# Optimization experiments

Measured on AMD Instinct MI355X. Metric: run time of the kernel, lower is better.

The kernel has to match this reference:

```python
import jax, jax.numpy as jnp
import numpy as np

D_MODEL = 512
NUM_HEADS = 8
D_K = D_MODEL // NUM_HEADS


def setup_inputs() -> dict:
    key = jax.random.key(0)
    ks = jax.random.split(key, 9)
    s = 1.0 / np.sqrt(D_MODEL)
    x = jax.random.normal(ks[0], (2, 4096, D_MODEL), dtype=jnp.float32)
    Wq = jax.random.uniform(ks[1], (D_MODEL, D_MODEL), jnp.float32, -s, s)
    bq = jax.random.uniform(ks[2], (D_MODEL,), jnp.float32, -s, s)
    Wk = jax.random.uniform(ks[3], (D_MODEL, D_MODEL), jnp.float32, -s, s)
    bk = jax.random.uniform(ks[4], (D_MODEL,), jnp.float32, -s, s)
    Wv = jax.random.uniform(ks[5], (D_MODEL, D_MODEL), jnp.float32, -s, s)
    bv = jax.random.uniform(ks[6], (D_MODEL,), jnp.float32, -s, s)
    Wo = jax.random.uniform(ks[7], (D_MODEL, D_MODEL), jnp.float32, -s, s)
    bo = jax.random.uniform(ks[8], (D_MODEL,), jnp.float32, -s, s)
    return {"x": x, "Wq": Wq, "bq": bq, "Wk": Wk, "bk": bk,
            "Wv": Wv, "bv": bv, "Wo": Wo, "bo": bo}


def reference(x, Wq, bq, Wk, bk, Wv, bv, Wo, bo):
    B, S, _ = x.shape
    # projections; split heads -> [B, H, S, d_k]
    def heads(t):
        return t.reshape(B, S, NUM_HEADS, D_K).transpose(0, 2, 1, 3)
    Q = heads(x @ Wq + bq)
    K = heads(x @ Wk + bk)
    V = heads(x @ Wv + bv)
    scores = jnp.einsum('bhqd,bhkd->bhqk', Q, K) / jnp.sqrt(jnp.float32(D_K))
    attn = jax.nn.softmax(scores, axis=-1)
    out = jnp.einsum('bhqk,bhkd->bhqd', attn, V)
    out = out.transpose(0, 2, 1, 3).reshape(B, S, D_MODEL)
    return out @ Wo + bo
```

## Files before the change

kernel.cpp:

```cpp
#include <hip/hip_runtime.h>
#include <hip/hip_bf16.h>

#define S_LEN 4096
#define DMODEL 512
#define NHEADS 8
#define DK 64
#define BATCH 2
#define MROWS (BATCH * S_LEN)

typedef __attribute__((ext_vector_type(8))) short bf16x8;
typedef __attribute__((ext_vector_type(4))) float f32x4;
typedef unsigned short ushort_t;

__device__ __forceinline__ unsigned packbf(float a, float b) {
  unsigned r;
  asm("v_cvt_pk_bf16_f32 %0, %1, %2" : "=v"(r) : "v"(a), "v"(b));
  return r;
}

__device__ __forceinline__ unsigned short bf1(float a) {
  union { __hip_bfloat16 h; unsigned short s; } u;
  u.h = __float2bfloat16(a);
  return u.s;
}

__device__ __forceinline__ void gll16(const void* g, void* l) {
  __builtin_amdgcn_global_load_lds(
      (const __attribute__((address_space(1))) unsigned*)g,
      (__attribute__((address_space(3))) unsigned*)l, 16, 0, 0);
}

__global__ __launch_bounds__(256) void cvt_bf16(const float* __restrict__ in,
                                                ushort_t* __restrict__ out) {
  size_t i = ((size_t)blockIdx.x * 256 + threadIdx.x) * 8;
  float4 a = *reinterpret_cast<const float4*>(in + i);
  float4 b = *reinterpret_cast<const float4*>(in + i + 4);
  uint4 o;
  o.x = packbf(a.x, a.y);
  o.y = packbf(a.z, a.w);
  o.z = packbf(b.x, b.y);
  o.w = packbf(b.z, b.w);
  *reinterpret_cast<uint4*>(out + i) = o;
}

__global__ __launch_bounds__(256) void transp_w(const float* __restrict__ W,
                                                ushort_t* __restrict__ Wt) {
  __shared__ float T[32][33];
  const int tid = threadIdx.x;
  const int k0 = blockIdx.x * 32, n0 = blockIdx.y * 32;
  const int r = tid >> 3, c4 = (tid & 7) * 4;
  float4 v = *reinterpret_cast<const float4*>(W + (size_t)(k0 + r) * 512 + n0 + c4);
  T[r][c4 + 0] = v.x; T[r][c4 + 1] = v.y; T[r][c4 + 2] = v.z; T[r][c4 + 3] = v.w;
  __syncthreads();
  uint2 o;
  o.x = packbf(T[c4 + 0][r], T[c4 + 1][r]);
  o.y = packbf(T[c4 + 2][r], T[c4 + 3][r]);
  *reinterpret_cast<uint2*>(Wt + (size_t)(n0 + r) * 512 + k0 + c4) = o;
}

__global__ __launch_bounds__(256) void gemm_qkv(
    const ushort_t* __restrict__ A, const ushort_t* __restrict__ Wcat,
    const float* __restrict__ bq, const float* __restrict__ bk,
    const float* __restrict__ bv, ushort_t* __restrict__ Qo,
    ushort_t* __restrict__ Ko, ushort_t* __restrict__ Vo, float CQ) {
  __shared__ ushort_t AL[2][128 * 32];
  __shared__ ushort_t BL[2][128 * 32];
  const int tid = threadIdx.x;
  const int wid = tid >> 6;
  const int lane = tid & 63;
  const int ql = lane & 15;
  const int g = lane >> 4;
  const int wr = wid >> 1, wc = wid & 1;
  const int m0 = blockIdx.x * 128, n0 = blockIdx.y * 128;
  const int region = n0 >> 9;

  f32x4 acc[4][4];
#pragma unroll
  for (int i = 0; i < 4; ++i)
#pragma unroll
    for (int j = 0; j < 4; ++j) acc[i][j] = (f32x4){0.f, 0.f, 0.f, 0.f};

  auto stage = [&](int k0, int buf) {
#pragma unroll
    for (int i = 0; i < 2; ++i) {
      int idx = i * 256 + tid;
      int r = idx >> 2;
      int c = (idx & 3) * 8;
      gll16(A + (size_t)(m0 + r) * 512 + k0 + c, &AL[buf][idx * 8]);
      gll16(Wcat + (size_t)(n0 + r) * 512 + k0 + c, &BL[buf][idx * 8]);
    }
  };

  stage(0, 0);
  __syncthreads();
  int buf = 0;

  for (int t = 0; t < 16; ++t) {
    if (t < 15) stage((t + 1) * 32, buf ^ 1);
    const ushort_t* ALb = &AL[buf][0];
    const ushort_t* BLb = &BL[buf][0];
    bf16x8 af[4], bfr[4];
#pragma unroll
    for (int mi = 0; mi < 4; ++mi)
      af[mi] = *reinterpret_cast<const bf16x8*>(ALb + (wr * 64 + mi * 16 + ql) * 32 + g * 8);
#pragma unroll
    for (int ni = 0; ni < 4; ++ni)
      bfr[ni] = *reinterpret_cast<const bf16x8*>(BLb + (wc * 64 + ni * 16 + ql) * 32 + g * 8);
#pragma unroll
    for (int mi = 0; mi < 4; ++mi)
#pragma unroll
      for (int ni = 0; ni < 4; ++ni)
        acc[mi][ni] = __builtin_amdgcn_mfma_f32_16x16x32_bf16(af[mi], bfr[ni], acc[mi][ni], 0, 0, 0);
    __syncthreads();
    buf ^= 1;
  }

  const float* bias = region == 0 ? bq : (region == 1 ? bk : bv);
  const float scale = region == 0 ? CQ : 1.0f;
  const int nl0 = n0 - (region << 9);
  ushort_t* outT = region == 0 ? Qo : Ko;

  float bvv[4];
#pragma unroll
  for (int ni = 0; ni < 4; ++ni) bvv[ni] = bias[nl0 + wc * 64 + ni * 16 + ql];

#pragma unroll
  for (int mi = 0; mi < 4; ++mi) {
#pragma unroll
    for (int ni = 0; ni < 4; ++ni) {
      int nl = nl0 + wc * 64 + ni * 16 + ql;
      int h = nl >> 6, d = nl & 63;
#pragma unroll
      for (int reg = 0; reg < 4; ++reg) {
        float val = (acc[mi][ni][reg] + bvv[ni]) * scale;
        int m = m0 + wr * 64 + mi * 16 + 4 * g + reg;
        int b = m >> 12, s = m & 4095;
        if (region <= 1) {
          outT[(((size_t)(b * NHEADS + h) * S_LEN + s) * DK) + d] = bf1(val);
        } else {
          int k6 = s & 63;
          int pos = (k6 & 32) | (((k6 >> 2) & 3) << 3) | (((k6 >> 4) & 1) << 2) | (k6 & 3);
          int sperm = (s & ~63) | pos;
          Vo[(((size_t)(b * NHEADS + h) * DK + d) * S_LEN) + sperm] = bf1(val);
        }
      }
    }
  }
}

__global__ __launch_bounds__(256) void gemm_wo(
    const ushort_t* __restrict__ A, const ushort_t* __restrict__ Wt,
    const float* __restrict__ bias, float* __restrict__ out) {
  __shared__ ushort_t AL[2][128 * 32];
  __shared__ ushort_t BL[2][128 * 32];
  const int tid = threadIdx.x;
  const int wid = tid >> 6;
  const int lane = tid & 63;
  const int ql = lane & 15;
  const int g = lane >> 4;
  const int wr = wid >> 1, wc = wid & 1;
  const int m0 = blockIdx.x * 128, n0 = blockIdx.y * 128;

  f32x4 acc[4][4];
#pragma unroll
  for (int i = 0; i < 4; ++i)
#pragma unroll
    for (int j = 0; j < 4; ++j) acc[i][j] = (f32x4){0.f, 0.f, 0.f, 0.f};

  auto stage = [&](int k0, int buf) {
#pragma unroll
    for (int i = 0; i < 2; ++i) {
      int idx = i * 256 + tid;
      int r = idx >> 2;
      int c = (idx & 3) * 8;
      gll16(A + (size_t)(m0 + r) * 512 + k0 + c, &AL[buf][idx * 8]);
      gll16(Wt + (size_t)(n0 + r) * 512 + k0 + c, &BL[buf][idx * 8]);
    }
  };

  stage(0, 0);
  __syncthreads();
  int buf = 0;

  for (int t = 0; t < 16; ++t) {
    if (t < 15) stage((t + 1) * 32, buf ^ 1);
    const ushort_t* ALb = &AL[buf][0];
    const ushort_t* BLb = &BL[buf][0];
    bf16x8 af[4], bfr[4];
#pragma unroll
    for (int mi = 0; mi < 4; ++mi)
      af[mi] = *reinterpret_cast<const bf16x8*>(ALb + (wr * 64 + mi * 16 + ql) * 32 + g * 8);
#pragma unroll
    for (int ni = 0; ni < 4; ++ni)
      bfr[ni] = *reinterpret_cast<const bf16x8*>(BLb + (wc * 64 + ni * 16 + ql) * 32 + g * 8);
#pragma unroll
    for (int mi = 0; mi < 4; ++mi)
#pragma unroll
      for (int ni = 0; ni < 4; ++ni)
        acc[mi][ni] = __builtin_amdgcn_mfma_f32_16x16x32_bf16(af[mi], bfr[ni], acc[mi][ni], 0, 0, 0);
    __syncthreads();
    buf ^= 1;
  }

  float bv[4];
#pragma unroll
  for (int ni = 0; ni < 4; ++ni) bv[ni] = bias[n0 + wc * 64 + ni * 16 + ql];

#pragma unroll
  for (int mi = 0; mi < 4; ++mi) {
#pragma unroll
    for (int ni = 0; ni < 4; ++ni) {
      int n = n0 + wc * 64 + ni * 16 + ql;
#pragma unroll
      for (int reg = 0; reg < 4; ++reg) {
        int m = m0 + wr * 64 + mi * 16 + 4 * g + reg;
        out[(size_t)m * 512 + n] = acc[mi][ni][reg] + bv[ni];
      }
    }
  }
}

template <bool SPLIT2>
__global__ __launch_bounds__(256, 4) void attn_mfma(
    const ushort_t* __restrict__ Q, const ushort_t* __restrict__ K,
    const ushort_t* __restrict__ Vt, ushort_t* __restrict__ AO,
    float* __restrict__ Opart, float* __restrict__ Lpart) {
  __shared__ ushort_t KL[2][64 * 64];
  __shared__ ushort_t VL[2][64 * 64];

  const int tid = threadIdx.x;
  const int wid = tid >> 6;
  const int lane = tid & 63;
  const int g = lane >> 4;
  const int ql = lane & 15;

  int L;
  if (SPLIT2) {
    int orig = blockIdx.x;
    L = (orig & 7) * 128 + (orig >> 3);
  } else {
    L = blockIdx.x;
  }
  const int qt = L & 31;
  const int bhsp = L >> 5;
  const int sp = SPLIT2 ? (bhsp & 1) : 0;
  const int bh = SPLIT2 ? (bhsp >> 1) : bhsp;
  const int NT = SPLIT2 ? 32 : 64;
  const int t0 = sp * NT;

  const ushort_t* Qb = Q + (size_t)bh * S_LEN * DK;
  const ushort_t* Kb = K + (size_t)bh * S_LEN * DK;
  const ushort_t* Vb = Vt + (size_t)bh * DK * S_LEN;

  const int qbase = qt * 128 + wid * 32;

  bf16x8 qf[2][2];
#pragma unroll
  for (int c = 0; c < 2; ++c) {
    int q = qbase + c * 16 + ql;
#pragma unroll
    for (int t = 0; t < 2; ++t)
      qf[c][t] = *reinterpret_cast<const bf16x8*>(Qb + (size_t)q * DK + t * 32 + g * 8);
  }

  bf16x8 ones;
#pragma unroll
  for (int j = 0; j < 8; ++j) ones[j] = (short)0x3F80;

  f32x4 ot[4][2];
#pragma unroll
  for (int db = 0; db < 4; ++db)
#pragma unroll
    for (int c = 0; c < 2; ++c) ot[db][c] = (f32x4){0.f, 0.f, 0.f, 0.f};
  f32x4 lacc[2];
  lacc[0] = (f32x4){0.f, 0.f, 0.f, 0.f};
  lacc[1] = (f32x4){0.f, 0.f, 0.f, 0.f};

  const int srow = lane >> 3;
  const int schk = lane & 7;
  const int r0 = wid * 16 + srow;
  const int r1 = r0 + 8;
  const int ssc = (schk ^ srow) << 4;

  const char* gk0 = (const char*)Kb + ((size_t)(t0 * 64 + r0)) * 128 + ssc;
  const char* gk1 = (const char*)Kb + ((size_t)(t0 * 64 + r1)) * 128 + ssc;
  const char* gv0 = (const char*)Vb + (size_t)r0 * (S_LEN * 2) + (size_t)t0 * 128 + ssc;
  const char* gv1 = (const char*)Vb + (size_t)r1 * (S_LEN * 2) + (size_t)t0 * 128 + ssc;

  char* lkA0 = (char*)&KL[0][0] + (wid * 16) * 128 + lane * 16;
  char* lkB0 = lkA0 + 8 * 128;
  char* lkA1 = lkA0 + 8192;
  char* lkB1 = lkB0 + 8192;
  char* lvA0 = (char*)&VL[0][0] + (wid * 16) * 128 + lane * 16;
  char* lvB0 = lvA0 + 8 * 128;
  char* lvA1 = lvA0 + 8192;
  char* lvB1 = lvB0 + 8192;

  int koA[4], koB[4];
#pragma unroll
  for (int kb = 0; kb < 4; ++kb) {
    int r = kb * 16 + ql;
    koA[kb] = r * 128 + (((g) ^ (r & 7)) << 4);
    koB[kb] = r * 128 + (((g + 4) ^ (r & 7)) << 4);
  }
  int voP[2][4];
#pragma unroll
  for (int t = 0; t < 2; ++t)
#pragma unroll
    for (int db = 0; db < 4; ++db) {
      int rd = db * 16 + ql;
      voP[t][db] = rd * 128 + (((t * 4 + g) ^ (rd & 7)) << 4);
    }

  gll16(gk0, lkA0); gll16(gk1, lkB0);
  gll16(gv0, lvA0); gll16(gv1, lvB0);
  gk0 += 8192; gk1 += 8192; gv0 += 128; gv1 += 128;
  __syncthreads();

  auto body = [&](const char* KB, const char* VB, char* dkA, char* dkB,
                  char* dvA, char* dvB, bool pref) {
    if (pref) {
      gll16(gk0, dkA); gll16(gk1, dkB);
      gll16(gv0, dvA); gll16(gv1, dvB);
      gk0 += 8192; gk1 += 8192; gv0 += 128; gv1 += 128;
    }

    f32x4 st[4][2];
    __builtin_amdgcn_s_setprio(1);
#pragma unroll
    for (int kb = 0; kb < 4; ++kb) {
      bf16x8 k0 = *reinterpret_cast<const bf16x8*>(KB + koA[kb]);
      bf16x8 k1 = *reinterpret_cast<const bf16x8*>(KB + koB[kb]);
#pragma unroll
      for (int c = 0; c < 2; ++c) {
        f32x4 z = (f32x4){0.f, 0.f, 0.f, 0.f};
        z = __builtin_amdgcn_mfma_f32_16x16x32_bf16(k0, qf[c][0], z, 0, 0, 0);
        z = __builtin_amdgcn_mfma_f32_16x16x32_bf16(k1, qf[c][1], z, 0, 0, 0);
        st[kb][c] = z;
      }
    }
    __builtin_amdgcn_s_setprio(0);

    unsigned pk[2][4][2];
#pragma unroll
    for (int c = 0; c < 2; ++c)
#pragma unroll
      for (int kb = 0; kb < 4; ++kb)
#pragma unroll
        for (int r2 = 0; r2 < 2; ++r2) {
          float pa = __builtin_amdgcn_exp2f(st[kb][c][2 * r2]);
          float pb_ = __builtin_amdgcn_exp2f(st[kb][c][2 * r2 + 1]);
          pk[c][kb][r2] = packbf(pa, pb_);
        }

    __builtin_amdgcn_s_setprio(1);
#pragma unroll
    for (int t = 0; t < 2; ++t) {
      union { unsigned u[4]; bf16x8 v; } pb0, pb1;
      pb0.u[0] = pk[0][2 * t][0];     pb0.u[1] = pk[0][2 * t][1];
      pb0.u[2] = pk[0][2 * t + 1][0]; pb0.u[3] = pk[0][2 * t + 1][1];
      pb1.u[0] = pk[1][2 * t][0];     pb1.u[1] = pk[1][2 * t][1];
      pb1.u[2] = pk[1][2 * t + 1][0]; pb1.u[3] = pk[1][2 * t + 1][1];
#pragma unroll
      for (int db = 0; db < 4; ++db) {
        bf16x8 af = *reinterpret_cast<const bf16x8*>(VB + voP[t][db]);
        ot[db][0] = __builtin_amdgcn_mfma_f32_16x16x32_bf16(af, pb0.v, ot[db][0], 0, 0, 0);
        ot[db][1] = __builtin_amdgcn_mfma_f32_16x16x32_bf16(af, pb1.v, ot[db][1], 0, 0, 0);
      }
      lacc[0] = __builtin_amdgcn_mfma_f32_16x16x32_bf16(ones, pb0.v, lacc[0], 0, 0, 0);
      lacc[1] = __builtin_amdgcn_mfma_f32_16x16x32_bf16(ones, pb1.v, lacc[1], 0, 0, 0);
    }
    __builtin_amdgcn_s_setprio(0);

    __syncthreads();
  };

  const char* KB0 = (const char*)&KL[0][0];
  const char* VB0 = (const char*)&VL[0][0];
  const char* KB1 = (const char*)&KL[1][0];
  const char* VB1 = (const char*)&VL[1][0];

  for (int it = 0; it < NT; it += 2) {
    body(KB0, VB0, lkA1, lkB1, lvA1, lvB1, true);
    body(KB1, VB1, lkA0, lkB0, lvA0, lvB0, it + 2 < NT);
  }

  if (SPLIT2) {
    float* Ob = Opart + (((size_t)sp * 16 + bh) * S_LEN) * 64;
#pragma unroll
    for (int c = 0; c < 2; ++c) {
      const int q = qbase + c * 16 + ql;
#pragma unroll
      for (int db = 0; db < 4; ++db) {
        float4 o = make_float4(ot[db][c][0], ot[db][c][1], ot[db][c][2], ot[db][c][3]);
        *reinterpret_cast<float4*>(Ob + (size_t)q * 64 + db * 16 + 4 * g) = o;
      }
      if (g == 0) Lpart[((size_t)sp * 16 + bh) * S_LEN + q] = lacc[c][0];
    }
  } else {
    const int b = bh >> 3, h = bh & 7;
#pragma unroll
    for (int c = 0; c < 2; ++c) {
      const int q = qbase + c * 16 + ql;
      float inv = 1.f / lacc[c][0];
#pragma unroll
      for (int db = 0; db < 4; ++db) {
        uint2 o;
        o.x = packbf(ot[db][c][0] * inv, ot[db][c][1] * inv);
        o.y = packbf(ot[db][c][2] * inv, ot[db][c][3] * inv);
        *reinterpret_cast<uint2*>(AO + ((size_t)b * S_LEN + q) * DMODEL + h * DK + db * 16 + g * 4) = o;
      }
    }
  }
}

__global__ __launch_bounds__(256) void combine_o(
    const float* __restrict__ Opart, const float* __restrict__ Lpart,
    ushort_t* __restrict__ AO) {
  int idx = blockIdx.x * 256 + threadIdx.x;
  int dblk = idx & 7;
  int q = (idx >> 3) & 4095;
  int bh = idx >> 15;
  size_t o0 = ((size_t)bh * S_LEN + q) * 64 + dblk * 8;
  size_t o1 = o0 + (size_t)16 * S_LEN * 64;
  float4 a0 = *reinterpret_cast<const float4*>(Opart + o0);
  float4 b0 = *reinterpret_cast<const float4*>(Opart + o0 + 4);
  float4 a1 = *reinterpret_cast<const float4*>(Opart + o1);
  float4 b1 = *reinterpret_cast<const float4*>(Opart + o1 + 4);
  float l = Lpart[(size_t)bh * S_LEN + q] + Lpart[(size_t)(16 + bh) * S_LEN + q];
  float inv = 1.0f / l;
  int b = bh >> 3, h = bh & 7;
  uint4 o;
  o.x = packbf((a0.x + a1.x) * inv, (a0.y + a1.y) * inv);
  o.y = packbf((a0.z + a1.z) * inv, (a0.w + a1.w) * inv);
  o.z = packbf((b0.x + b1.x) * inv, (b0.y + b1.y) * inv);
  o.w = packbf((b0.z + b1.z) * inv, (b0.w + b1.w) * inv);
  *reinterpret_cast<uint4*>(AO + ((size_t)b * S_LEN + q) * DMODEL + h * 64 + dblk * 8) = o;
}

extern "C" void kernel_launch(void* const* d_in, const int* in_sizes, int n_in,
                              void* d_out, int out_size, void* d_ws, size_t ws_size,
                              hipStream_t stream) {
  const float* x  = (const float*)d_in[0];
  const float* Wq = (const float*)d_in[1];
  const float* bq = (const float*)d_in[2];
  const float* Wk = (const float*)d_in[3];
  const float* bk = (const float*)d_in[4];
  const float* Wv = (const float*)d_in[5];
  const float* bv = (const float*)d_in[6];
  const float* Wo = (const float*)d_in[7];
  const float* bo = (const float*)d_in[8];
  float* out = (float*)d_out;

  const float CQ = 0.18033688f;

  char* ws = (char*)d_ws;
  const size_t NBF = (size_t)MROWS * DMODEL;
  ushort_t* xbf = (ushort_t*)ws;
  ushort_t* Qbf = (ushort_t*)(ws + NBF * 2);
  ushort_t* Kbf = (ushort_t*)(ws + NBF * 4);
  ushort_t* Vtb = (ushort_t*)(ws + NBF * 6);

  const size_t OFF_WT    = NBF * 8;
  const size_t OFF_LPART = OFF_WT + 4 * 512 * 512 * 2;
  const size_t OFF_OPART = OFF_LPART + 512 * 1024;
  const size_t NEED_SPLIT = OFF_OPART + (size_t)2 * 16 * S_LEN * 64 * 4;
  const bool use_split = ws_size >= NEED_SPLIT;

  ushort_t* Wcat;
  ushort_t* AOb;
  if (use_split) {
    Wcat = (ushort_t*)(ws + OFF_WT);
    AOb = xbf;
  } else {
    AOb = (ushort_t*)(ws + NBF * 8);
    Wcat = (ushort_t*)(ws + NBF * 10);
  }
  ushort_t* Wot = Wcat + 3 * 512 * 512;
  float* Lpart = (float*)(ws + OFF_LPART);
  float* Opart = (float*)(ws + OFF_OPART);

  cvt_bf16<<<MROWS * DMODEL / 2048, 256, 0, stream>>>(x, xbf);
  dim3 gt(16, 16);
  transp_w<<<gt, 256, 0, stream>>>(Wq, Wcat);
  transp_w<<<gt, 256, 0, stream>>>(Wk, Wcat + 512 * 512);
  transp_w<<<gt, 256, 0, stream>>>(Wv, Wcat + 2 * 512 * 512);
  transp_w<<<gt, 256, 0, stream>>>(Wo, Wot);

  dim3 gq(MROWS / 128, 1536 / 128);
  gemm_qkv<<<gq, 256, 0, stream>>>(xbf, Wcat, bq, bk, bv, Qbf, Kbf, Vtb, CQ);

  if (use_split) {
    attn_mfma<true><<<1024, 256, 0, stream>>>(Qbf, Kbf, Vtb, AOb, Opart, Lpart);
    combine_o<<<2048, 256, 0, stream>>>(Opart, Lpart, AOb);
  } else {
    attn_mfma<false><<<512, 256, 0, stream>>>(Qbf, Kbf, Vtb, AOb, Opart, Lpart);
  }

  dim3 gg(MROWS / 128, DMODEL / 128);
  gemm_wo<<<gg, 256, 0, stream>>>(AOb, Wot, bo, out);
}
```

Measured before the change: 127.9 us.

## Fuse split-KV combine into output GEMM, bf16 partials, merged prep kernel, XCD block remap

Removes the separate combine kernel by having the output-projection GEMM load both bf16 attention partials, sum them, normalise by the summed row sums and stage the result into LDS as its A operand. Attention partials are now stored in bf16 instead of fp32, halving that intermediate traffic. The x conversion and four weight transposes become one launch. The QKV and output GEMM grids are remapped so neighbouring tiles land on the same XCD. In exchange, the A operand is loaded through registers rather than direct-to-LDS, and the partials lose precision before the combine.

```diff
diff --git a/kernel.cpp b/kernel.cpp
--- a/kernel.cpp
+++ b/kernel.cpp
@@ -24,38 +24,55 @@
   return u.s;
 }
 
+__device__ __forceinline__ float bflo(unsigned u) { return __uint_as_float(u << 16); }
+__device__ __forceinline__ float bfhi(unsigned u) { return __uint_as_float(u & 0xFFFF0000u); }
+
+__device__ __forceinline__ float fastrcp(float x) {
+  float r;
+  asm("v_rcp_f32 %0, %1" : "=v"(r) : "v"(x));
+  return r;
+}
+
 __device__ __forceinline__ void gll16(const void* g, void* l) {
   __builtin_amdgcn_global_load_lds(
       (const __attribute__((address_space(1))) unsigned*)g,
       (__attribute__((address_space(3))) unsigned*)l, 16, 0, 0);
 }
 
-__global__ __launch_bounds__(256) void cvt_bf16(const float* __restrict__ in,
-                                                ushort_t* __restrict__ out) {
-  size_t i = ((size_t)blockIdx.x * 256 + threadIdx.x) * 8;
-  float4 a = *reinterpret_cast<const float4*>(in + i);
-  float4 b = *reinterpret_cast<const float4*>(in + i + 4);
-  uint4 o;
-  o.x = packbf(a.x, a.y);
-  o.y = packbf(a.z, a.w);
-  o.z = packbf(b.x, b.y);
-  o.w = packbf(b.z, b.w);
-  *reinterpret_cast<uint4*>(out + i) = o;
-}
-
-__global__ __launch_bounds__(256) void transp_w(const float* __restrict__ W,
-                                                ushort_t* __restrict__ Wt) {
+__global__ __launch_bounds__(256) void prep(
+    const float* __restrict__ x, const float* __restrict__ Wq,
+    const float* __restrict__ Wk, const float* __restrict__ Wv,
+    const float* __restrict__ Wo, ushort_t* __restrict__ xbf,
+    ushort_t* __restrict__ Wcat, ushort_t* __restrict__ Wot) {
   __shared__ float T[32][33];
+  const int bid = blockIdx.x;
   const int tid = threadIdx.x;
-  const int k0 = blockIdx.x * 32, n0 = blockIdx.y * 32;
-  const int r = tid >> 3, c4 = (tid & 7) * 4;
-  float4 v = *reinterpret_cast<const float4*>(W + (size_t)(k0 + r) * 512 + n0 + c4);
-  T[r][c4 + 0] = v.x; T[r][c4 + 1] = v.y; T[r][c4 + 2] = v.z; T[r][c4 + 3] = v.w;
-  __syncthreads();
-  uint2 o;
-  o.x = packbf(T[c4 + 0][r], T[c4 + 1][r]);
-  o.y = packbf(T[c4 + 2][r], T[c4 + 3][r]);
-  *reinterpret_cast<uint2*>(Wt + (size_t)(n0 + r) * 512 + k0 + c4) = o;
+  if (bid < 2048) {
+    size_t i = ((size_t)bid * 256 + tid) * 8;
+    float4 a = *reinterpret_cast<const float4*>(x + i);
+    float4 b = *reinterpret_cast<const float4*>(x + i + 4);
+    uint4 o;
+    o.x = packbf(a.x, a.y);
+    o.y = packbf(a.z, a.w);
+    o.z = packbf(b.x, b.y);
+    o.w = packbf(b.z, b.w);
+    *reinterpret_cast<uint4*>(xbf + i) = o;
+  } else {
+    int t = bid - 2048;
+    int w = t >> 8;
+    int tile = t & 255;
+    int k0 = (tile & 15) * 32, n0 = (tile >> 4) * 32;
+    const float* W = w == 0 ? Wq : (w == 1 ? Wk : (w == 2 ? Wv : Wo));
+    ushort_t* out = (w == 3) ? Wot : (Wcat + (size_t)w * 512 * 512);
+    const int r = tid >> 3, c4 = (tid & 7) * 4;
+    float4 v = *reinterpret_cast<const float4*>(W + (size_t)(k0 + r) * 512 + n0 + c4);
+    T[r][c4 + 0] = v.x; T[r][c4 + 1] = v.y; T[r][c4 + 2] = v.z; T[r][c4 + 3] = v.w;
+    __syncthreads();
+    uint2 o;
+    o.x = packbf(T[c4 + 0][r], T[c4 + 1][r]);
+    o.y = packbf(T[c4 + 2][r], T[c4 + 3][r]);
+    *reinterpret_cast<uint2*>(out + (size_t)(n0 + r) * 512 + k0 + c4) = o;
+  }
 }
 
 __global__ __launch_bounds__(256) void gemm_qkv(
@@ -71,7 +88,12 @@
   const int ql = lane & 15;
   const int g = lane >> 4;
   const int wr = wid >> 1, wc = wid & 1;
-  const int m0 = blockIdx.x * 128, n0 = blockIdx.y * 128;
+
+  const int p = blockIdx.x;
+  const int xcd = p & 7, q_ = p >> 3;
+  const int mi = xcd * 8 + q_ / 12;
+  const int ni = q_ % 12;
+  const int m0 = mi * 128, n0 = ni * 128;
   const int region = n0 >> 9;
 
   f32x4 acc[4][4];
@@ -101,16 +123,16 @@
     const ushort_t* BLb = &BL[buf][0];
     bf16x8 af[4], bfr[4];
 #pragma unroll
-    for (int mi = 0; mi < 4; ++mi)
-      af[mi] = *reinterpret_cast<const bf16x8*>(ALb + (wr * 64 + mi * 16 + ql) * 32 + g * 8);
-#pragma unroll
-    for (int ni = 0; ni < 4; ++ni)
-      bfr[ni] = *reinterpret_cast<const bf16x8*>(BLb + (wc * 64 + ni * 16 + ql) * 32 + g * 8);
-#pragma unroll
-    for (int mi = 0; mi < 4; ++mi)
-#pragma unroll
-      for (int ni = 0; ni < 4; ++ni)
-        acc[mi][ni] = __builtin_amdgcn_mfma_f32_16x16x32_bf16(af[mi], bfr[ni], acc[mi][ni], 0, 0, 0);
+    for (int mi2 = 0; mi2 < 4; ++mi2)
+      af[mi2] = *reinterpret_cast<const bf16x8*>(ALb + (wr * 64 + mi2 * 16 + ql) * 32 + g * 8);
+#pragma unroll
+    for (int ni2 = 0; ni2 < 4; ++ni2)
+      bfr[ni2] = *reinterpret_cast<const bf16x8*>(BLb + (wc * 64 + ni2 * 16 + ql) * 32 + g * 8);
+#pragma unroll
+    for (int mi2 = 0; mi2 < 4; ++mi2)
+#pragma unroll
+      for (int ni2 = 0; ni2 < 4; ++ni2)
+        acc[mi2][ni2] = __builtin_amdgcn_mfma_f32_16x16x32_bf16(af[mi2], bfr[ni2], acc[mi2][ni2], 0, 0, 0);
     __syncthreads();
     buf ^= 1;
   }
@@ -122,18 +144,18 @@
 
   float bvv[4];
 #pragma unroll
-  for (int ni = 0; ni < 4; ++ni) bvv[ni] = bias[nl0 + wc * 64 + ni * 16 + ql];
-
-#pragma unroll
-  for (int mi = 0; mi < 4; ++mi) {
-#pragma unroll
-    for (int ni = 0; ni < 4; ++ni) {
-      int nl = nl0 + wc * 64 + ni * 16 + ql;
+  for (int ni2 = 0; ni2 < 4; ++ni2) bvv[ni2] = bias[nl0 + wc * 64 + ni2 * 16 + ql];
+
+#pragma unroll
+  for (int mi2 = 0; mi2 < 4; ++mi2) {
+#pragma unroll
+    for (int ni2 = 0; ni2 < 4; ++ni2) {
+      int nl = nl0 + wc * 64 + ni2 * 16 + ql;
       int h = nl >> 6, d = nl & 63;
 #pragma unroll
       for (int reg = 0; reg < 4; ++reg) {
-        float val = (acc[mi][ni][reg] + bvv[ni]) * scale;
-        int m = m0 + wr * 64 + mi * 16 + 4 * g + reg;
+        float val = (acc[mi2][ni2][reg] + bvv[ni2]) * scale;
+        int m = m0 + wr * 64 + mi2 * 16 + 4 * g + reg;
         int b = m >> 12, s = m & 4095;
         if (region <= 1) {
           outT[(((size_t)(b * NHEADS + h) * S_LEN + s) * DK) + d] = bf1(val);
@@ -143,6 +165,134 @@
           int sperm = (s & ~63) | pos;
           Vo[(((size_t)(b * NHEADS + h) * DK + d) * S_LEN) + sperm] = bf1(val);
         }
+      }
+    }
+  }
+}
+
+__global__ __launch_bounds__(256) void gemm_wo_fused(
+    const ushort_t* __restrict__ Opart, const float* __restrict__ Lpart,
+    const ushort_t* __restrict__ Wt, const float* __restrict__ bias,
+    float* __restrict__ out) {
+  __shared__ ushort_t AL[2][128 * 32];
+  __shared__ ushort_t BL[2][128 * 32];
+  const int tid = threadIdx.x;
+  const int wid = tid >> 6;
+  const int lane = tid & 63;
+  const int ql = lane & 15;
+  const int g = lane >> 4;
+  const int wr = wid >> 1, wc = wid & 1;
+
+  const int p = blockIdx.x;
+  const int L = (p & 7) * 32 + (p >> 3);
+  const int m0 = (L >> 2) * 128, n0 = (L & 3) * 128;
+
+  f32x4 acc[4][4];
+#pragma unroll
+  for (int i = 0; i < 4; ++i)
+#pragma unroll
+    for (int j = 0; j < 4; ++j) acc[i][j] = (f32x4){0.f, 0.f, 0.f, 0.f};
+
+  const int r_[2] = {tid >> 2, 256 / 4 + (tid >> 2)};
+  const int c8 = (tid & 3) * 8;
+
+  int sA[2], bhbase[2];
+#pragma unroll
+  for (int i = 0; i < 2; ++i) {
+    int m = m0 + r_[i];
+    int b = m >> 12;
+    sA[i] = m & 4095;
+    bhbase[i] = b * 8;
+  }
+
+  auto loadA = [&](int k0, uint4 av[2], float inv[2]) {
+    int kg = k0 + c8;
+    int h = kg >> 6, d = kg & 63;
+#pragma unroll
+    for (int i = 0; i < 2; ++i) {
+      int bh = bhbase[i] + h;
+      size_t off = ((size_t)bh * S_LEN + sA[i]) * 64 + d;
+      av[i] = *reinterpret_cast<const uint4*>(Opart + off);
+      uint4 a1 = *reinterpret_cast<const uint4*>(Opart + off + (size_t)16 * S_LEN * 64);
+      float l = Lpart[(size_t)bh * S_LEN + sA[i]] + Lpart[((size_t)(16 + bh)) * S_LEN + sA[i]];
+      inv[i] = fastrcp(l);
+      unsigned u0[4] = {av[i].x, av[i].y, av[i].z, av[i].w};
+      unsigned u1[4] = {a1.x, a1.y, a1.z, a1.w};
+      unsigned r[4];
+#pragma unroll
+      for (int j = 0; j < 4; ++j) {
+        float e0 = (bflo(u0[j]) + bflo(u1[j])) * inv[i];
+        float e1 = (bfhi(u0[j]) + bfhi(u1[j])) * inv[i];
+        r[j] = packbf(e0, e1);
+      }
+      av[i].x = r[0]; av[i].y = r[1]; av[i].z = r[2]; av[i].w = r[3];
+    }
+  };
+
+  auto writeA = [&](int buf, uint4 av[2]) {
+#pragma unroll
+    for (int i = 0; i < 2; ++i) {
+      int idx = i * 256 + tid;
+      *reinterpret_cast<uint4*>(&AL[buf][idx * 8]) = av[i];
+    }
+  };
+
+  auto stageB = [&](int k0, int buf) {
+#pragma unroll
+    for (int i = 0; i < 2; ++i) {
+      int idx = i * 256 + tid;
+      int r = idx >> 2;
+      int c = (idx & 3) * 8;
+      gll16(Wt + (size_t)(n0 + r) * 512 + k0 + c, &BL[buf][idx * 8]);
+    }
+  };
+
+  {
+    uint4 av[2]; float inv[2];
+    loadA(0, av, inv);
+    writeA(0, av);
+    stageB(0, 0);
+  }
+  __syncthreads();
+
+  for (int t = 0; t < 16; ++t) {
+    const int buf = t & 1;
+    uint4 av[2]; float inv[2];
+    if (t < 15) {
+      stageB((t + 1) * 32, buf ^ 1);
+      loadA((t + 1) * 32, av, inv);
+    }
+    const ushort_t* ALb = &AL[buf][0];
+    const ushort_t* BLb = &BL[buf][0];
+    bf16x8 af[4], bfr[4];
+#pragma unroll
+    for (int mi = 0; mi < 4; ++mi)
+      af[mi] = *reinterpret_cast<const bf16x8*>(ALb + (wr * 64 + mi * 16 + ql) * 32 + g * 8);
+#pragma unroll
+    for (int ni = 0; ni < 4; ++ni)
+      bfr[ni] = *reinterpret_cast<const bf16x8*>(BLb + (wc * 64 + ni * 16 + ql) * 32 + g * 8);
+#pragma unroll
+    for (int mi = 0; mi < 4; ++mi)
+#pragma unroll
+      for (int ni = 0; ni < 4; ++ni)
+        acc[mi][ni] = __builtin_amdgcn_mfma_f32_16x16x32_bf16(af[mi], bfr[ni], acc[mi][ni], 0, 0, 0);
+    if (t < 15) writeA(buf ^ 1, av);
+    __syncthreads();
+  }
+
+  float bv[4];
+#pragma unroll
+  for (int ni = 0; ni < 4; ++ni) bv[ni] = bias[n0 + wc * 64 + ni * 16 + ql];
+
+#pragma unroll
+  for (int mi = 0; mi < 4; ++mi) {
+#pragma unroll
+    for (int ni = 0; ni < 4; ++ni) {
+      int n = n0 + wc * 64 + ni * 16 + ql;
+#pragma unroll
+      for (int reg = 0; reg < 4; ++reg) {
+        int m = m0 + wr * 64 + mi * 16 + 4 * g + reg;
+        out[(size_t)m * 512 + n] = acc[mi][ni][reg] + bv[ni];
       }
     }
   }
@@ -224,7 +374,7 @@
 __global__ __launch_bounds__(256, 4) void attn_mfma(
     const ushort_t* __restrict__ Q, const ushort_t* __restrict__ K,
     const ushort_t* __restrict__ Vt, ushort_t* __restrict__ AO,
-    float* __restrict__ Opart, float* __restrict__ Lpart) {
+    ushort_t* __restrict__ Opart, float* __restrict__ Lpart) {
   __shared__ ushort_t KL[2][64 * 64];
   __shared__ ushort_t VL[2][64 * 64];
 
@@ -386,14 +536,16 @@
   }
 
   if (SPLIT2) {
-    float* Ob = Opart + (((size_t)sp * 16 + bh) * S_LEN) * 64;
+    ushort_t* Ob = Opart + (((size_t)sp * 16 + bh) * S_LEN) * 64;
 #pragma unroll
     for (int c = 0; c < 2; ++c) {
       const int q = qbase + c * 16 + ql;
 #pragma unroll
       for (int db = 0; db < 4; ++db) {
-        float4 o = make_float4(ot[db][c][0], ot[db][c][1], ot[db][c][2], ot[db][c][3]);
-        *reinterpret_cast<float4*>(Ob + (size_t)q * 64 + db * 16 + 4 * g) = o;
+        uint2 o;
+        o.x = packbf(ot[db][c][0], ot[db][c][1]);
+        o.y = packbf(ot[db][c][2], ot[db][c][3]);
+        *reinterpret_cast<uint2*>(Ob + (size_t)q * 64 + db * 16 + 4 * g) = o;
       }
       if (g == 0) Lpart[((size_t)sp * 16 + bh) * S_LEN + q] = lacc[c][0];
     }
@@ -412,30 +564,6 @@
       }
     }
   }
-}
-
-__global__ __launch_bounds__(256) void combine_o(
-    const float* __restrict__ Opart, const float* __restrict__ Lpart,
-    ushort_t* __restrict__ AO) {
-  int idx = blockIdx.x * 256 + threadIdx.x;
-  int dblk = idx & 7;
-  int q = (idx >> 3) & 4095;
-  int bh = idx >> 15;
-  size_t o0 = ((size_t)bh * S_LEN + q) * 64 + dblk * 8;
-  size_t o1 = o0 + (size_t)16 * S_LEN * 64;
-  float4 a0 = *reinterpret_cast<const float4*>(Opart + o0);
-  float4 b0 = *reinterpret_cast<const float4*>(Opart + o0 + 4);
-  float4 a1 = *reinterpret_cast<const float4*>(Opart + o1);
-  float4 b1 = *reinterpret_cast<const float4*>(Opart + o1 + 4);
-  float l = Lpart[(size_t)bh * S_LEN + q] + Lpart[(size_t)(16 + bh) * S_LEN + q];
-  float inv = 1.0f / l;
-  int b = bh >> 3, h = bh & 7;
-  uint4 o;
-  o.x = packbf((a0.x + a1.x) * inv, (a0.y + a1.y) * inv);
-  o.y = packbf((a0.z + a1.z) * inv, (a0.w + a1.w) * inv);
-  o.z = packbf((b0.x + b1.x) * inv, (b0.y + b1.y) * inv);
-  o.w = packbf((b0.z + b1.z) * inv, (b0.w + b1.w) * inv);
-  *reinterpret_cast<uint4*>(AO + ((size_t)b * S_LEN + q) * DMODEL + h * 64 + dblk * 8) = o;
 }
 
 extern "C" void kernel_launch(void* const* d_in, const int* in_sizes, int n_in,
@@ -464,7 +592,7 @@
   const size_t OFF_WT    = NBF * 8;
   const size_t OFF_LPART = OFF_WT + 4 * 512 * 512 * 2;
   const size_t OFF_OPART = OFF_LPART + 512 * 1024;
-  const size_t NEED_SPLIT = OFF_OPART + (size_t)2 * 16 * S_LEN * 64 * 4;
+  const size_t NEED_SPLIT = OFF_OPART + (size_t)2 * 16 * S_LEN * 64 * 2;
   const bool use_split = ws_size >= NEED_SPLIT;
 
   ushort_t* Wcat;
@@ -478,25 +606,18 @@
   }
   ushort_t* Wot = Wcat + 3 * 512 * 512;
   float* Lpart = (float*)(ws + OFF_LPART);
-  float* Opart = (float*)(ws + OFF_OPART);
-
-  cvt_bf16<<<MROWS * DMODEL / 2048, 256, 0, stream>>>(x, xbf);
-  dim3 gt(16, 16);
-  transp_w<<<gt, 256, 0, stream>>>(Wq, Wcat);
-  transp_w<<<gt, 256, 0, stream>>>(Wk, Wcat + 512 * 512);
-  transp_w<<<gt, 256, 0, stream>>>(Wv, Wcat + 2 * 512 * 512);
-  transp_w<<<gt, 256, 0, stream>>>(Wo, Wot);
-
-  dim3 gq(MROWS / 128, 1536 / 128);
-  gemm_qkv<<<gq, 256, 0, stream>>>(xbf, Wcat, bq, bk, bv, Qbf, Kbf, Vtb, CQ);
+  ushort_t* Opart = (ushort_t*)(ws + OFF_OPART);
+
+  prep<<<3072, 256, 0, stream>>>(x, Wq, Wk, Wv, Wo, xbf, Wcat, Wot);
+
+  gemm_qkv<<<768, 256, 0, stream>>>(xbf, Wcat, bq, bk, bv, Qbf, Kbf, Vtb, CQ);
 
   if (use_split) {
     attn_mfma<true><<<1024, 256, 0, stream>>>(Qbf, Kbf, Vtb, AOb, Opart, Lpart);
-    combine_o<<<2048, 256, 0, stream>>>(Opart, Lpart, AOb);
+    gemm_wo_fused<<<256, 256, 0, stream>>>(Opart, Lpart, Wot, bo, out);
   } else {
     attn_mfma<false><<<512, 256, 0, stream>>>(Qbf, Kbf, Vtb, AOb, Opart, Lpart);
-  }
-
-  dim3 gg(MROWS / 128, DMODEL / 128);
-  gemm_wo<<<gg, 256, 0, stream>>>(AOb, Wot, bo, out);
-}
+    dim3 gg(MROWS / 128, DMODEL / 128);
+    gemm_wo<<<gg, 256, 0, stream>>>(AOb, Wot, bo, out);
+  }
+}
```

Result: faster. 122.4 us (-4.3%).
